# Kernel tuning notes

Hardware: AMD Instinct MI355X
Metric: run time of the kernel (lower is better)

Reference implementation:

```python
import jax, jax.numpy as jnp
import numpy as np

DIM, QS, NH, WS, SS, FFW = 256, 56, 8, 7, 3, 1024


def _make_attn_mask(H, W, ws, ss):
    # Swin-style shifted-window attention mask, [nWin, ws*ws, ws*ws]
    img = np.zeros((H, W))
    cnt = 0
    for hs in (slice(0, -ws), slice(-ws, -ss), slice(-ss, None)):
        for wsl in (slice(0, -ws), slice(-ws, -ss), slice(-ss, None)):
            img[hs, wsl] = cnt
            cnt += 1
    mw = img.reshape(H // ws, ws, W // ws, ws).transpose(0, 2, 1, 3).reshape(-1, ws * ws)
    am = mw[:, None, :] - mw[:, :, None]
    return jnp.asarray(np.where(am != 0, -100.0, 0.0), jnp.float32)

ATTN_MASK = _make_attn_mask(QS, QS, WS, SS)


def setup_inputs() -> dict:
    key = jax.random.key(0)
    ks = jax.random.split(key, 16)
    s = lambda fan: 1.0 / np.sqrt(fan)
    return {
        'x': jax.random.normal(ks[0], (16, DIM, QS, QS), jnp.float32),
        'ln1_g': jnp.ones((DIM,), jnp.float32),
        'ln1_b': jnp.zeros((DIM,), jnp.float32),
        'ln2_g': jnp.ones((DIM,), jnp.float32),
        'ln2_b': jnp.zeros((DIM,), jnp.float32),
        'qkv_w': jax.random.normal(ks[1], (DIM, 3 * DIM), jnp.float32) * s(DIM),
        'qkv_b': jnp.zeros((3 * DIM,), jnp.float32),
        'proj_w': jax.random.normal(ks[2], (DIM, DIM), jnp.float32) * s(DIM),
        'proj_b': jnp.zeros((DIM,), jnp.float32),
        'ffn_w1': jax.random.normal(ks[3], (DIM, FFW), jnp.float32) * s(DIM),
        'ffn_b1': jnp.zeros((FFW,), jnp.float32),
        'ffn_w2': jax.random.normal(ks[4], (FFW, DIM), jnp.float32) * s(FFW),
        'ffn_b2': jnp.zeros((DIM,), jnp.float32),
        'layer_scale': jax.random.normal(ks[5], (DIM,), jnp.float32),
    }


def _ln(t, g, b):
    m = t.mean(-1, keepdims=True)
    v = ((t - m) ** 2).mean(-1, keepdims=True)
    return (t - m) * jax.lax.rsqrt(v + 1e-5) * g + b


def reference(x, ln1_g, ln1_b, ln2_g, ln2_b, qkv_w, qkv_b, proj_w, proj_b,
              ffn_w1, ffn_b1, ffn_w2, ffn_b2, layer_scale):
    B, C, H, W = x.shape
    nh, ws, ss = NH, WS, SS
    hd = C // nh
    nHw, nWw = H // ws, W // ws
    xh = jnp.transpose(x, (0, 2, 3, 1))  # B H W C

    # --- shifted window attention ---
    h = _ln(xh, ln1_g, ln1_b)
    h = jnp.roll(h, (-ss, -ss), axis=(1, 2))
    # window partition: [B, nWin, L, C]
    h = h.reshape(B, nHw, ws, nWw, ws, C).transpose(0, 1, 3, 2, 4, 5)
    h = h.reshape(B, nHw * nWw, ws * ws, C)
    qkv = h @ qkv_w + qkv_b
    q, k, v = jnp.split(qkv, 3, axis=-1)
    L = ws * ws
    q = q.reshape(B, -1, L, nh, hd).transpose(0, 1, 3, 2, 4)  # B W h L d
    k = k.reshape(B, -1, L, nh, hd).transpose(0, 1, 3, 2, 4)
    v = v.reshape(B, -1, L, nh, hd).transpose(0, 1, 3, 2, 4)
    attn = jnp.einsum('bwhid,bwhjd->bwhij', q, k) * (hd ** -0.5)
    attn = attn + ATTN_MASK[None, :, None]  # mask per window index
    attn = jax.nn.softmax(attn, axis=-1)
    o = jnp.einsum('bwhij,bwhjd->bwhid', attn, v)
    o = o.transpose(0, 1, 3, 2, 4).reshape(B, nHw * nWw, L, C)
    o = o @ proj_w + proj_b
    # reverse partition + roll back
    o = o.reshape(B, nHw, nWw, ws, ws, C).transpose(0, 1, 3, 2, 4, 5).reshape(B, H, W, C)
    o = jnp.roll(o, (ss, ss), axis=(1, 2))
    x1 = xh + o

    # --- FFN ---
    h2 = _ln(x1, ln2_g, ln2_b)
    f = jax.nn.relu(h2 @ ffn_w1 + ffn_b1) @ ffn_w2 + ffn_b2
    f = f * layer_scale
    out = x1 + f
    return jnp.transpose(out, (0, 3, 1, 2))  # back to B C H W
```

## Files before the change

kernel.cpp:

```cpp
#include <hip/hip_runtime.h>
#include <hip/hip_bf16.h>
#include <math.h>

typedef unsigned short u16;
typedef __bf16 bf16x8 __attribute__((ext_vector_type(8)));
typedef float  f32x4  __attribute__((ext_vector_type(4)));

#define DIMC 256
#define QSZ  56
#define WSZ  7
#define SSZ  3
#define LWIN 49
#define NWIN 64
#define HW   3136
#define NTOK 50176
#define FFWD 1024
#define FCH  25088

__device__ __forceinline__ u16 f2bu(float f) {
    __hip_bfloat16 h = __float2bfloat16(f);
    return __builtin_bit_cast(u16, h);
}
__device__ __forceinline__ float bu2f(u16 u) {
    unsigned v = (unsigned)u << 16;
    return __builtin_bit_cast(float, v);
}
__device__ __forceinline__ void gload_lds16(const void* g, void* l) {
    __builtin_amdgcn_global_load_lds((const __attribute__((address_space(1))) void*)g,
                                     (__attribute__((address_space(3))) void*)l, 16, 0, 0);
}

__device__ __forceinline__ int region_of(int h) {
    return (h < 49) ? 0 : ((h < 53) ? 1 : 2);
}

__device__ __forceinline__ int row2tok(int m) {
    int b  = m / (NWIN * LWIN);
    int r  = m - b * (NWIN * LWIN);
    int wi = r / LWIN;
    int p  = r - wi * LWIN;
    int wh = wi >> 3, ww = wi & 7;
    int ph = p / 7,   pw = p - ph * 7;
    int hr = wh * 7 + ph, wr = ww * 7 + pw;
    int hs = hr + SSZ; if (hs >= QSZ) hs -= QSZ;
    int ws2 = wr + SSZ; if (ws2 >= QSZ) ws2 -= QSZ;
    return b * HW + hs * QSZ + ws2;
}

__device__ __forceinline__ void wconv_body(const float* __restrict__ W,
        u16* __restrict__ Wt, int K, int N, int bx, int by, int t) {
    __shared__ float tile[32][33];
    int k0 = bx * 32, n0 = by * 32;
    int tx = t & 31, ty = t >> 5;
    for (int kk = ty; kk < 32; kk += 8)
        tile[kk][tx] = W[(size_t)(k0 + kk) * N + n0 + tx];
    __syncthreads();
    for (int nn = ty; nn < 32; nn += 8)
        Wt[(size_t)(n0 + nn) * K + k0 + tx] = f2bu(tile[tx][nn]);
}

__global__ __launch_bounds__(256) void k_wconv_all(
        const float* __restrict__ qkv_w, u16* __restrict__ wqt,
        const float* __restrict__ proj_w, u16* __restrict__ wpt,
        const float* __restrict__ ffn_w1, u16* __restrict__ w1t,
        const float* __restrict__ ffn_w2, u16* __restrict__ w2t) {
    int b = blockIdx.x, t = threadIdx.x;
    if (b < 192)        wconv_body(qkv_w, wqt, 256, 768, b & 7, b >> 3, t);
    else if (b < 256) { b -= 192; wconv_body(proj_w, wpt, 256, 256,  b & 7, b >> 3, t); }
    else if (b < 512) { b -= 256; wconv_body(ffn_w1, w1t, 256, 1024, b & 7, b >> 3, t); }
    else              { b -= 512; wconv_body(ffn_w2, w2t, 1024, 256, b & 31, b >> 5, t); }
}

__global__ __launch_bounds__(256) void k_ln1(const float* __restrict__ x,
        const float* __restrict__ g, const float* __restrict__ be,
        u16* __restrict__ hln) {
    __shared__ float tile[32][257];
    __shared__ float msh[32], rsh[32];
    int blk = blockIdx.x;
    int b   = blk / 98;
    int hw0 = (blk - b * 98) * 32;
    int t   = threadIdx.x;
    int tx  = t & 31, ty = t >> 5;
    for (int c = ty; c < 256; c += 8)
        tile[tx][c] = x[(size_t)(b * 256 + c) * HW + hw0 + tx];
    __syncthreads();
    int row = t >> 3, sub = t & 7;
    float s = 0.f, sq = 0.f;
    for (int c = sub * 32; c < sub * 32 + 32; ++c) {
        float v = tile[row][c]; s += v; sq += v * v;
    }
    for (int o = 4; o; o >>= 1) { s += __shfl_down(s, o, 8); sq += __shfl_down(sq, o, 8); }
    if (sub == 0) {
        float m   = s * (1.f / 256.f);
        float var = sq * (1.f / 256.f) - m * m;
        msh[row] = m; rsh[row] = rsqrtf(var + 1e-5f);
    }
    __syncthreads();
    float gg = g[t], bb = be[t];
    for (int r2 = 0; r2 < 32; ++r2) {
        float v = tile[r2][t];
        hln[(size_t)(b * HW + hw0 + r2) * 256 + t] = f2bu((v - msh[r2]) * rsh[r2] * gg + bb);
    }
}

__global__ __launch_bounds__(256) void k_ln2t(const float* __restrict__ x,
        u16* __restrict__ x1b, const float* __restrict__ g,
        const float* __restrict__ be, u16* __restrict__ h2) {
    __shared__ float tile[32][257];
    __shared__ float msh[32], rsh[32];
    int blk = blockIdx.x;
    int b   = blk / 98;
    int hw0 = (blk - b * 98) * 32;
    int t   = threadIdx.x;
    int tx  = t & 31, ty = t >> 5;
    for (int c = ty; c < 256; c += 8)
        tile[tx][c] = x[(size_t)(b * 256 + c) * HW + hw0 + tx];
    __syncthreads();
    size_t base = (size_t)b * HW + hw0;
    for (int r2 = 0; r2 < 32; ++r2) {
        float v = tile[r2][t] + bu2f(x1b[(base + r2) * 256 + t]);
        tile[r2][t] = v;
        x1b[(base + r2) * 256 + t] = f2bu(v);
    }
    __syncthreads();
    int row = t >> 3, sub = t & 7;
    float s = 0.f, sq = 0.f;
    for (int c = sub * 32; c < sub * 32 + 32; ++c) {
        float v = tile[row][c]; s += v; sq += v * v;
    }
    for (int o = 4; o; o >>= 1) { s += __shfl_down(s, o, 8); sq += __shfl_down(sq, o, 8); }
    if (sub == 0) {
        float m   = s * (1.f / 256.f);
        float var = sq * (1.f / 256.f) - m * m;
        msh[row] = m; rsh[row] = rsqrtf(var + 1e-5f);
    }
    __syncthreads();
    float gg = g[t], bb = be[t];
    for (int r2 = 0; r2 < 32; ++r2) {
        float v = tile[r2][t];
        h2[(base + r2) * 256 + t] = f2bu((v - msh[r2]) * rsh[r2] * gg + bb);
    }
}

template<int MODE>
__global__ __launch_bounds__(512) void k_mgemm256(
        const u16* __restrict__ A, const u16* __restrict__ Bt,
        const float* __restrict__ bias, void* __restrict__ Cv, int K, int N) {
    __shared__ __align__(16) u16 As[2][256 * 32];
    __shared__ __align__(16) u16 Bs[2][128 * 32];
    const int m0 = blockIdx.x * 256, n0 = blockIdx.y * 128;
    const int t = threadIdx.x, lane = t & 63;
    const int wv = t >> 6, wr = wv >> 1, wc = wv & 1;

    const int kc = (t & 3) ^ ((t >> 3) & 3);
    int ar0 = m0 + (t >> 2), ar1 = m0 + 128 + (t >> 2);
    if (MODE == 0) { ar0 = row2tok(ar0); ar1 = row2tok(ar1); }
    const u16* gA0 = A  + (size_t)ar0 * K + kc * 8;
    const u16* gA1 = A  + (size_t)ar1 * K + kc * 8;
    const u16* gB0 = Bt + (size_t)(n0 + (t >> 2)) * K + kc * 8;

    f32x4 acc[4][4] = {};
    const int ra = wr * 64 + (lane & 15);
    const int rb = wc * 64 + (lane & 15);
    const int kos = (((lane >> 4) ^ (lane >> 1)) & 3) * 8;
    const int nIter = K >> 5;

    gload_lds16(gA0, As[0] + t * 8);
    gload_lds16(gA1, As[0] + 4096 + t * 8);
    gload_lds16(gB0, Bs[0] + t * 8);

    int cur = 0;
    for (int it = 0; it < nIter; ++it) {
        if (it + 1 < nIter) {
            const int k1 = (it + 1) << 5;
            gload_lds16(gA0 + k1, As[cur ^ 1] + t * 8);
            gload_lds16(gA1 + k1, As[cur ^ 1] + 4096 + t * 8);
            gload_lds16(gB0 + k1, Bs[cur ^ 1] + t * 8);
            asm volatile("s_waitcnt vmcnt(3)" ::: "memory");
        } else {
            asm volatile("s_waitcnt vmcnt(0)" ::: "memory");
        }
        __builtin_amdgcn_s_barrier();
        __builtin_amdgcn_sched_barrier(0);
        bf16x8 af[4], bfr[4];
#pragma unroll
        for (int i = 0; i < 4; ++i)
            af[i] = *(const bf16x8*)(As[cur] + (ra + i * 16) * 32 + kos);
#pragma unroll
        for (int j = 0; j < 4; ++j)
            bfr[j] = *(const bf16x8*)(Bs[cur] + (rb + ((j & 1) * 16 + (j >> 1) * 32)) * 32 + kos);
        asm volatile("s_waitcnt lgkmcnt(0)" ::: "memory");
        __builtin_amdgcn_sched_barrier(0);
        __builtin_amdgcn_s_barrier();
#pragma unroll
        for (int i = 0; i < 4; ++i)
#pragma unroll
            for (int j = 0; j < 4; ++j)
                acc[i][j] = __builtin_amdgcn_mfma_f32_16x16x32_bf16(af[i], bfr[j], acc[i][j], 0, 0, 0);
        cur ^= 1;
    }

    const int rowb = m0 + wr * 64 + ((lane >> 4) * 4);
    u16* Cb = (u16*)Cv;
#pragma unroll
    for (int j = 0; j < 4; ++j) {
        int col = n0 + wc * 64 + ((j & 1) * 16 + (j >> 1) * 32) + (lane & 15);
        float bj = bias[col];
#pragma unroll
        for (int i = 0; i < 4; ++i) {
            int rw = rowb + i * 16;
#pragma unroll
            for (int r = 0; r < 4; ++r) {
                float v = acc[i][j][r] + bj;
                if (MODE == 2) v = fmaxf(v, 0.f);
                Cb[(size_t)(rw + r) * N + col] = f2bu(v);
            }
        }
    }
}

template<int MODE>
__global__ __launch_bounds__(256) void k_mgemm128(
        const u16* __restrict__ A, const u16* __restrict__ Bt,
        const float* __restrict__ bias, void* __restrict__ Cv,
        int K, int N, const void* __restrict__ extra,
        const float* __restrict__ extra2, int grow0) {
    __shared__ __align__(16) u16 As[2][128 * 32];
    __shared__ __align__(16) u16 Bs[2][128 * 32];
    const int m0 = blockIdx.x * 128, n0 = blockIdx.y * 128;
    const int t = threadIdx.x, lane = t & 63;
    const int wv = t >> 6, wr = wv >> 1, wc = wv & 1;

    const int kc = (t & 3) ^ ((t >> 3) & 3);
    const u16* gA0 = A  + (size_t)(m0 + (t >> 2)) * K + kc * 8;
    const u16* gA1 = A  + (size_t)(m0 + 64 + (t >> 2)) * K + kc * 8;
    const u16* gB0 = Bt + (size_t)(n0 + (t >> 2)) * K + kc * 8;
    const u16* gB1 = Bt + (size_t)(n0 + 64 + (t >> 2)) * K + kc * 8;

    f32x4 acc[4][4] = {};
    const int ra = wr * 64 + (lane & 15);
    const int rb = wc * 64 + (lane & 15);
    const int kos = (((lane >> 4) ^ (lane >> 1)) & 3) * 8;
    const int nIter = K >> 5;

    gload_lds16(gA0, As[0] + t * 8);
    gload_lds16(gA1, As[0] + 2048 + t * 8);
    gload_lds16(gB0, Bs[0] + t * 8);
    gload_lds16(gB1, Bs[0] + 2048 + t * 8);

    int cur = 0;
    for (int it = 0; it < nIter; ++it) {
        if (it + 1 < nIter) {
            const int k1 = (it + 1) << 5;
            gload_lds16(gA0 + k1, As[cur ^ 1] + t * 8);
            gload_lds16(gA1 + k1, As[cur ^ 1] + 2048 + t * 8);
            gload_lds16(gB0 + k1, Bs[cur ^ 1] + t * 8);
            gload_lds16(gB1 + k1, Bs[cur ^ 1] + 2048 + t * 8);
            asm volatile("s_waitcnt vmcnt(4)" ::: "memory");
        } else {
            asm volatile("s_waitcnt vmcnt(0)" ::: "memory");
        }
        __builtin_amdgcn_s_barrier();
        __builtin_amdgcn_sched_barrier(0);
        bf16x8 af[4], bfr[4];
#pragma unroll
        for (int i = 0; i < 4; ++i)
            af[i] = *(const bf16x8*)(As[cur] + (ra + i * 16) * 32 + kos);
#pragma unroll
        for (int j = 0; j < 4; ++j)
            bfr[j] = *(const bf16x8*)(Bs[cur] + (rb + j * 16) * 32 + kos);
        asm volatile("s_waitcnt lgkmcnt(0)" ::: "memory");
        __builtin_amdgcn_sched_barrier(0);
        __builtin_amdgcn_s_barrier();
#pragma unroll
        for (int i = 0; i < 4; ++i)
#pragma unroll
            for (int j = 0; j < 4; ++j)
                acc[i][j] = __builtin_amdgcn_mfma_f32_16x16x32_bf16(af[i], bfr[j], acc[i][j], 0, 0, 0);
        cur ^= 1;
    }

    const int colb = n0 + wc * 64 + (lane & 15);
    const int rowb = m0 + wr * 64 + ((lane >> 4) * 4);

    if constexpr (MODE == 1) {
        u16* Cb = (u16*)Cv;
        int tok[4][4];
#pragma unroll
        for (int i = 0; i < 4; ++i)
#pragma unroll
            for (int r = 0; r < 4; ++r)
                tok[i][r] = row2tok(rowb + i * 16 + r);
#pragma unroll
        for (int j = 0; j < 4; ++j) {
            int col = colb + j * 16; float bj = bias[col];
#pragma unroll
            for (int i = 0; i < 4; ++i)
#pragma unroll
                for (int r = 0; r < 4; ++r)
                    Cb[(size_t)tok[i][r] * 256 + col] = f2bu(acc[i][j][r] + bj);
        }
    } else {
        float* C = (float*)Cv;
        const u16* xr = (const u16*)extra;
#pragma unroll
        for (int j = 0; j < 4; ++j) {
            int col = colb + j * 16;
            float bj = bias[col], lj = extra2[col];
#pragma unroll
            for (int i = 0; i < 4; ++i) {
                int g  = grow0 + rowb + i * 16;
                int b  = g / HW, hw = g - b * HW;
                f32x4 o;
#pragma unroll
                for (int r = 0; r < 4; ++r)
                    o[r] = bu2f(xr[(size_t)(g + r) * 256 + col]) + lj * (acc[i][j][r] + bj);
                *(f32x4*)(C + ((size_t)(b * 256 + col)) * HW + hw) = o;
            }
        }
    }
}

__global__ __launch_bounds__(256, 4) void k_attn(const u16* __restrict__ qkv,
        u16* __restrict__ oattn) {
    __shared__ __align__(16) u16 Pl[4 * 49 * 72 + 15 * 72];
    const int wv = threadIdx.x >> 6, lane = threadIdx.x & 63;
    const int task = blockIdx.x * 4 + wv;
    const int head = task & 7, win = task >> 3, wi = win & 63;
    const int rowbase = win * LWIN;
    const int g = lane >> 4, c = lane & 15, ko = g * 8;
    const u16* qb = qkv + (size_t)rowbase * 768 + head * 32;
    u16* pl = Pl + wv * (49 * 72);

    bf16x8 vb[2][2];
#pragma unroll
    for (int j2 = 0; j2 < 2; ++j2) {
        int d = j2 * 16 + c;
#pragma unroll
        for (int h = 0; h < 2; ++h)
#pragma unroll
            for (int tt = 0; tt < 8; ++tt) {
                int k = h * 32 + ko + tt;
                u16 val = (k < LWIN) ? qb[(size_t)k * 768 + 512 + d] : (u16)0;
                vb[j2][h][tt] = __builtin_bit_cast(__bf16, val);
            }
    }

    bf16x8 qf[4], kf[4];
#pragma unroll
    for (int i = 0; i < 4; ++i) {
        int r0 = i * 16 + c; if (r0 > 48) r0 = 48;
        qf[i] = *(const bf16x8*)(qb + (size_t)r0 * 768 + ko);
        kf[i] = *(const bf16x8*)(qb + (size_t)r0 * 768 + 256 + ko);
    }
    f32x4 s[4][4] = {};
    __builtin_amdgcn_s_setprio(1);
#pragma unroll
    for (int i = 0; i < 4; ++i)
#pragma unroll
        for (int j = 0; j < 4; ++j)
            s[i][j] = __builtin_amdgcn_mfma_f32_16x16x32_bf16(qf[i], kf[j], s[i][j], 0, 0, 0);
    __builtin_amdgcn_s_setprio(0);

    const int wh7 = (wi >> 3) * 7, ww7 = (wi & 7) * 7;
    int idj[4]; bool jok[4];
#pragma unroll
    for (int j = 0; j < 4; ++j) {
        int col = j * 16 + c;
        jok[j] = col < LWIN;
        int p = jok[j] ? col : 48;
        idj[j] = region_of(wh7 + p / 7) * 3 + region_of(ww7 + p % 7);
    }
#pragma unroll
    for (int i = 0; i < 4; ++i) {
#pragma unroll
        for (int r = 0; r < 4; ++r) {
            int row = i * 16 + g * 4 + r;
            int p = row < LWIN ? row : 48;
            int idi = region_of(wh7 + p / 7) * 3 + region_of(ww7 + p % 7);
            float mx = -1e30f;
#pragma unroll
            for (int j = 0; j < 4; ++j) {
                float tv = jok[j] ? fmaf(s[i][j][r], 0.17677669529663687f,
                                         (idi == idj[j]) ? 0.f : -100.f)
                                  : -1e30f;
                s[i][j][r] = tv;
                mx = fmaxf(mx, tv);
            }
            for (int o = 8; o; o >>= 1) mx = fmaxf(mx, __shfl_xor(mx, o));
            float ps = 0.f;
#pragma unroll
            for (int j = 0; j < 4; ++j) {
                float e = __expf(s[i][j][r] - mx);
                s[i][j][r] = e; ps += e;
            }
            for (int o = 8; o; o >>= 1) ps += __shfl_xor(ps, o);
            float inv = 1.f / ps;
            if (row < LWIN) {
#pragma unroll
                for (int j = 0; j < 4; ++j)
                    pl[row * 72 + j * 16 + c] = f2bu(s[i][j][r] * inv);
            }
        }
    }

    f32x4 o[4][2] = {};
    __builtin_amdgcn_s_setprio(1);
#pragma unroll
    for (int i = 0; i < 4; ++i) {
        bf16x8 pa0 = *(const bf16x8*)(&pl[(i * 16 + c) * 72 + ko]);
        bf16x8 pa1 = *(const bf16x8*)(&pl[(i * 16 + c) * 72 + ko + 32]);
#pragma unroll
        for (int j2 = 0; j2 < 2; ++j2) {
            o[i][j2] = __builtin_amdgcn_mfma_f32_16x16x32_bf16(pa0, vb[j2][0], o[i][j2], 0, 0, 0);
            o[i][j2] = __builtin_amdgcn_mfma_f32_16x16x32_bf16(pa1, vb[j2][1], o[i][j2], 0, 0, 0);
        }
    }
    __builtin_amdgcn_s_setprio(0);
#pragma unroll
    for (int i = 0; i < 4; ++i)
#pragma unroll
        for (int r = 0; r < 4; ++r) {
            int row = i * 16 + g * 4 + r;
            if (row < LWIN) {
#pragma unroll
                for (int j2 = 0; j2 < 2; ++j2)
                    oattn[(size_t)(rowbase + row) * 256 + head * 32 + j2 * 16 + c]
                        = f2bu(o[i][j2][r]);
            }
        }
}

extern "C" void kernel_launch(void* const* d_in, const int* in_sizes, int n_in,
                              void* d_out, int out_size, void* d_ws, size_t ws_size,
                              hipStream_t stream) {
    const float* x      = (const float*)d_in[0];
    const float* ln1_g  = (const float*)d_in[1];
    const float* ln1_b  = (const float*)d_in[2];
    const float* ln2_g  = (const float*)d_in[3];
    const float* ln2_b  = (const float*)d_in[4];
    const float* qkv_w  = (const float*)d_in[5];
    const float* qkv_b  = (const float*)d_in[6];
    const float* proj_w = (const float*)d_in[7];
    const float* proj_b = (const float*)d_in[8];
    const float* ffn_w1 = (const float*)d_in[9];
    const float* ffn_b1 = (const float*)d_in[10];
    const float* ffn_w2 = (const float*)d_in[11];
    const float* ffn_b2 = (const float*)d_in[12];
    const float* lscale = (const float*)d_in[13];

    char* wsb = (char*)d_ws;
    u16* wqt  = (u16*)(wsb);
    u16* wpt  = (u16*)(wsb + 393216);
    u16* w1t  = (u16*)(wsb + 524288);
    u16* w2t  = (u16*)(wsb + 1048576);
    u16* P    = (u16*)(wsb + 1572864);
    char* Qb  = wsb + 27262976;
    u16* qkvb = (u16*)Qb;
    u16* x1b  = (u16*)Qb;
    u16* f1c  = (u16*)(Qb + 25690112);

    k_wconv_all<<<768, 256, 0, stream>>>(qkv_w, wqt, proj_w, wpt, ffn_w1, w1t, ffn_w2, w2t);

    k_ln1<<<16 * 98, 256, 0, stream>>>(x, ln1_g, ln1_b, P);
    k_mgemm256<0><<<dim3(196, 6), 512, 0, stream>>>(P, wqt, qkv_b, qkvb, 256, 768);
    k_attn<<<2048, 256, 0, stream>>>(qkvb, P);
    k_mgemm128<1><<<dim3(392, 2), 256, 0, stream>>>(P, wpt, proj_b, x1b, 256, 256,
                                                    nullptr, nullptr, 0);
    k_ln2t<<<16 * 98, 256, 0, stream>>>(x, x1b, ln2_g, ln2_b, P);
    for (int c = 0; c < 2; ++c) {
        k_mgemm256<2><<<dim3(98, 8), 512, 0, stream>>>(P + (size_t)c * FCH * 256, w1t, ffn_b1,
                                                       f1c, 256, 1024);
        k_mgemm128<3><<<dim3(196, 2), 256, 0, stream>>>(f1c, w2t, ffn_b2, d_out, 1024, 256,
                                                        x1b, lscale, c * FCH);
    }
}
```

Measured before the change: 272.5 us.

## Fuse window attention with output projection GEMM in one kernel

Merges the window attention kernel and the projection GEMM into a single kernel. Each 512-thread block handles one window, with one wave per head, and stages the attention output in LDS. The block then streams the projection weights through double-buffered LDS and runs MFMA to write x1 directly. This removes the global round trip of the attention output and one kernel launch. In exchange, every window reloads the full 256x256 projection weight, and the larger LDS footprint may lower occupancy.

```diff
diff --git a/kernel.cpp b/kernel.cpp
--- a/kernel.cpp
+++ b/kernel.cpp
@@ -283,54 +283,35 @@
     const int colb = n0 + wc * 64 + (lane & 15);
     const int rowb = m0 + wr * 64 + ((lane >> 4) * 4);
 
-    if constexpr (MODE == 1) {
-        u16* Cb = (u16*)Cv;
-        int tok[4][4];
-#pragma unroll
-        for (int i = 0; i < 4; ++i)
+    float* C = (float*)Cv;
+    const u16* xr = (const u16*)extra;
+#pragma unroll
+    for (int j = 0; j < 4; ++j) {
+        int col = colb + j * 16;
+        float bj = bias[col], lj = extra2[col];
+#pragma unroll
+        for (int i = 0; i < 4; ++i) {
+            int g  = grow0 + rowb + i * 16;
+            int b  = g / HW, hw = g - b * HW;
+            f32x4 o;
 #pragma unroll
             for (int r = 0; r < 4; ++r)
-                tok[i][r] = row2tok(rowb + i * 16 + r);
-#pragma unroll
-        for (int j = 0; j < 4; ++j) {
-            int col = colb + j * 16; float bj = bias[col];
-#pragma unroll
-            for (int i = 0; i < 4; ++i)
-#pragma unroll
-                for (int r = 0; r < 4; ++r)
-                    Cb[(size_t)tok[i][r] * 256 + col] = f2bu(acc[i][j][r] + bj);
-        }
-    } else {
-        float* C = (float*)Cv;
-        const u16* xr = (const u16*)extra;
-#pragma unroll
-        for (int j = 0; j < 4; ++j) {
-            int col = colb + j * 16;
-            float bj = bias[col], lj = extra2[col];
-#pragma unroll
-            for (int i = 0; i < 4; ++i) {
-                int g  = grow0 + rowb + i * 16;
-                int b  = g / HW, hw = g - b * HW;
-                f32x4 o;
-#pragma unroll
-                for (int r = 0; r < 4; ++r)
-                    o[r] = bu2f(xr[(size_t)(g + r) * 256 + col]) + lj * (acc[i][j][r] + bj);
-                *(f32x4*)(C + ((size_t)(b * 256 + col)) * HW + hw) = o;
-            }
-        }
-    }
-}
-
-__global__ __launch_bounds__(256, 4) void k_attn(const u16* __restrict__ qkv,
-        u16* __restrict__ oattn) {
-    __shared__ __align__(16) u16 Pl[4 * 49 * 72 + 15 * 72];
+                o[r] = bu2f(xr[(size_t)(g + r) * 256 + col]) + lj * (acc[i][j][r] + bj);
+            *(f32x4*)(C + ((size_t)(b * 256 + col)) * HW + hw) = o;
+        }
+    }
+}
+
+__global__ __launch_bounds__(512) void k_attnproj(const u16* __restrict__ qkv,
+        const u16* __restrict__ wpt, const float* __restrict__ pbias,
+        u16* __restrict__ x1b) {
+    __shared__ __align__(16) u16 U[33280];
     const int wv = threadIdx.x >> 6, lane = threadIdx.x & 63;
-    const int task = blockIdx.x * 4 + wv;
-    const int head = task & 7, win = task >> 3, wi = win & 63;
+    const int win = blockIdx.x, head = wv, wi = win & 63;
     const int rowbase = win * LWIN;
     const int g = lane >> 4, c = lane & 15, ko = g * 8;
     const u16* qb = qkv + (size_t)rowbase * 768 + head * 32;
-    u16* pl = Pl + wv * (49 * 72);
+    u16* pl = U + wv * (LWIN * 72);
 
     bf16x8 vb[2][2];
 #pragma unroll
@@ -417,6 +398,17 @@
         }
     }
     __builtin_amdgcn_s_setprio(0);
+
+    __syncthreads();
+
+    u16* o_t = U;
+    u16* wst = U + 16896;
+    {
+        int cidx = threadIdx.x, n = cidx >> 2, sub = cidx & 3;
+        gload_lds16(wpt + (size_t)n * 256 + (sub ^ ((n >> 1) & 3)) * 8, wst + cidx * 8);
+        cidx += 512; n = cidx >> 2; sub = cidx & 3;
+        gload_lds16(wpt + (size_t)n * 256 + (sub ^ ((n >> 1) & 3)) * 8, wst + cidx * 8);
+    }
 #pragma unroll
     for (int i = 0; i < 4; ++i)
 #pragma unroll
@@ -425,10 +417,64 @@
             if (row < LWIN) {
 #pragma unroll
                 for (int j2 = 0; j2 < 2; ++j2)
-                    oattn[(size_t)(rowbase + row) * 256 + head * 32 + j2 * 16 + c]
-                        = f2bu(o[i][j2][r]);
-            }
-        }
+                    o_t[row * 264 + head * 32 + j2 * 16 + c] = f2bu(o[i][j2][r]);
+            }
+        }
+    __syncthreads();
+
+    f32x4 acc2[4][2] = {};
+    const int kos2 = ((g ^ (lane >> 1)) & 3) * 8;
+    int curb = 0;
+    for (int it = 0; it < 8; ++it) {
+        if (it + 1 < 8) {
+            int kc0 = (it + 1) * 32;
+            int cidx = threadIdx.x, n = cidx >> 2, sub = cidx & 3;
+            gload_lds16(wpt + (size_t)n * 256 + kc0 + (sub ^ ((n >> 1) & 3)) * 8,
+                        wst + (curb ^ 1) * 8192 + cidx * 8);
+            cidx += 512; n = cidx >> 2; sub = cidx & 3;
+            gload_lds16(wpt + (size_t)n * 256 + kc0 + (sub ^ ((n >> 1) & 3)) * 8,
+                        wst + (curb ^ 1) * 8192 + cidx * 8);
+            asm volatile("s_waitcnt vmcnt(2)" ::: "memory");
+        } else {
+            asm volatile("s_waitcnt vmcnt(0)" ::: "memory");
+        }
+        __builtin_amdgcn_s_barrier();
+        __builtin_amdgcn_sched_barrier(0);
+        bf16x8 af[4], bf2[2];
+#pragma unroll
+        for (int i = 0; i < 4; ++i)
+            af[i] = *(const bf16x8*)(o_t + (i * 16 + c) * 264 + it * 32 + ko);
+#pragma unroll
+        for (int j2 = 0; j2 < 2; ++j2)
+            bf2[j2] = *(const bf16x8*)(wst + curb * 8192 + (wv * 32 + j2 * 16 + c) * 32 + kos2);
+        asm volatile("s_waitcnt lgkmcnt(0)" ::: "memory");
+        __builtin_amdgcn_sched_barrier(0);
+        __builtin_amdgcn_s_barrier();
+        __builtin_amdgcn_s_setprio(1);
+#pragma unroll
+        for (int i = 0; i < 4; ++i)
+#pragma unroll
+            for (int j2 = 0; j2 < 2; ++j2)
+                acc2[i][j2] = __builtin_amdgcn_mfma_f32_16x16x32_bf16(af[i], bf2[j2], acc2[i][j2], 0, 0, 0);
+        __builtin_amdgcn_s_setprio(0);
+        curb ^= 1;
+    }
+
+#pragma unroll
+    for (int j2 = 0; j2 < 2; ++j2) {
+        int col = wv * 32 + j2 * 16 + c;
+        float bj = pbias[col];
+#pragma unroll
+        for (int i = 0; i < 4; ++i)
+#pragma unroll
+            for (int r = 0; r < 4; ++r) {
+                int row = i * 16 + g * 4 + r;
+                if (row < LWIN) {
+                    int tok = row2tok(rowbase + row);
+                    x1b[(size_t)tok * 256 + col] = f2bu(acc2[i][j2][r] + bj);
+                }
+            }
+    }
 }
 
 extern "C" void kernel_launch(void* const* d_in, const int* in_sizes, int n_in,
@@ -464,9 +510,7 @@
 
     k_ln1<<<16 * 98, 256, 0, stream>>>(x, ln1_g, ln1_b, P);
     k_mgemm256<0><<<dim3(196, 6), 512, 0, stream>>>(P, wqt, qkv_b, qkvb, 256, 768);
-    k_attn<<<2048, 256, 0, stream>>>(qkvb, P);
-    k_mgemm128<1><<<dim3(392, 2), 256, 0, stream>>>(P, wpt, proj_b, x1b, 256, 256,
-                                                    nullptr, nullptr, 0);
+    k_attnproj<<<1024, 512, 0, stream>>>(qkvb, wpt, proj_b, x1b);
     k_ln2t<<<16 * 98, 256, 0, stream>>>(x, x1b, ln2_g, ln2_b, P);
     for (int c = 0; c < 2; ++c) {
         k_mgemm256<2><<<dim3(98, 8), 512, 0, stream>>>(P + (size_t)c * FCH * 256, w1t, ffn_b1,
```

Result: no change. 269.7 us (-1.0%).
